# Kernel optimization log

Measured on AMD Instinct MI355X. Metric: run time of the kernel, lower is better.

The kernel has to match this reference:

```python
import jax, jax.numpy as jnp
import numpy as np
import math

C, NH, HD, L, P, FFN = 256, 8, 32, 1, 4, 512
H_BEV, W_BEV = 200, 100
NQ, BS, NV = 1000, 4, H_BEV * W_BEV
EPS = 1e-5


def _ln(x, g, b):
    m = x.mean(-1, keepdims=True)
    v = ((x - m) ** 2).mean(-1, keepdims=True)
    return (x - m) / jnp.sqrt(v + EPS) * g + b


def _mha(x, qpos, in_w, in_b, ow, ob):
    # nn.MultiheadAttention self-attention; key_pos = query_pos (shapes match)
    q = x + qpos
    k = x + qpos
    v = x
    wq, wk, wv = jnp.split(in_w, 3, axis=0)
    bq, bk, bv = jnp.split(in_b, 3, axis=0)
    bs, nq, _ = x.shape
    qh = (q @ wq.T + bq).reshape(bs, nq, NH, HD)
    kh = (k @ wk.T + bk).reshape(bs, nq, NH, HD)
    vh = (v @ wv.T + bv).reshape(bs, nq, NH, HD)
    scores = jnp.einsum('bqhd,bkhd->bhqk', qh, kh) / jnp.sqrt(jnp.float32(HD))
    attn = jax.nn.softmax(scores, axis=-1)
    out = jnp.einsum('bhqk,bkhd->bqhd', attn, vh).reshape(bs, nq, C)
    return out @ ow.T + ob


def _msdeform(x, qpos, value, ref, spatial_shapes, so_w, so_b, aw_w, aw_b, vp_w, vp_b, op_w, op_b):
    # Multi-scale deformable attention (single level), bilinear sampling with
    # align_corners=False convention and zero padding, as in the CUDA kernel.
    bs, nq, _ = x.shape
    q = x + qpos
    v = (value @ vp_w.T + vp_b).reshape(bs, NV, NH, HD).transpose(0, 2, 1, 3)  # [bs,nh,nv,hd]
    off = (q @ so_w.T + so_b).reshape(bs, nq, NH, L, P, 2)
    aw = jax.nn.softmax((q @ aw_w.T + aw_b).reshape(bs, nq, NH, L * P), axis=-1)
    aw = aw.reshape(bs, nq, NH, L, P)
    norm = jnp.stack([spatial_shapes[:, 1], spatial_shapes[:, 0]], -1).astype(jnp.float32)  # [L,2] = (W,H)
    loc = ref[:, :, None, :, None, :] + off / norm[None, None, None, :, None, :]  # [bs,nq,nh,L,P,2]
    loc = loc[:, :, :, 0]  # single level -> [bs,nq,nh,P,2]
    awp = aw[:, :, :, 0]   # [bs,nq,nh,P]
    x_im = loc[..., 0] * W_BEV - 0.5
    y_im = loc[..., 1] * H_BEV - 0.5
    x0 = jnp.floor(x_im)
    y0 = jnp.floor(y_im)
    lx = x_im - x0
    ly = y_im - y0
    x0i = x0.astype(jnp.int32)
    y0i = y0.astype(jnp.int32)
    acc = jnp.zeros((bs, NH, nq, P, HD), jnp.float32)
    for dy in (0, 1):
        for dx in (0, 1):
            xi = x0i + dx
            yi = y0i + dy
            w = (lx if dx else 1.0 - lx) * (ly if dy else 1.0 - ly)  # [bs,nq,nh,P]
            ok = ((xi >= 0) & (xi < W_BEV) & (yi >= 0) & (yi < H_BEV)).astype(jnp.float32)
            idx = jnp.clip(yi, 0, H_BEV - 1) * W_BEV + jnp.clip(xi, 0, W_BEV - 1)
            idx_t = idx.transpose(0, 2, 1, 3).reshape(bs, NH, nq * P)
            g = jnp.take_along_axis(v, idx_t[..., None], axis=2).reshape(bs, NH, nq, P, HD)
            acc = acc + g * (w * ok).transpose(0, 2, 1, 3)[..., None]
    out = (acc * awp.transpose(0, 2, 1, 3)[..., None]).sum(3)  # [bs,nh,nq,hd]
    out = out.transpose(0, 2, 1, 3).reshape(bs, nq, C)
    return out @ op_w.T + op_b


def setup_inputs() -> dict:
    key = jax.random.key(0)
    ks = jax.random.split(key, 24)
    f32 = jnp.float32

    def w(k, shp):
        fan = shp[-1]
        return (jax.random.normal(k, shp, f32) * (1.0 / np.sqrt(fan))).astype(f32)

    # sampling_offsets bias per _reset_parameters (radial grid init)
    thetas = np.arange(NH, dtype=np.float32) * (2.0 * math.pi / NH)
    grid = np.stack([np.cos(thetas), np.sin(thetas)], -1)
    grid = grid / np.abs(grid).max(-1, keepdims=True)
    grid = np.tile(grid[:, None, None, :], (1, L, P, 1))
    for i in range(P):
        grid[:, :, i, :] *= i + 1
    so_b = jnp.asarray(grid.reshape(-1), f32)

    return {
        'query': jax.random.normal(ks[0], (NQ, BS, C), f32),
        'value': jax.random.normal(ks[1], (NV, BS, C), f32),
        'query_pos': jax.random.normal(ks[2], (NQ, BS, C), f32),
        'reference_points': jax.random.uniform(ks[3], (BS, NQ, L, 2), f32),
        'spatial_shapes': jnp.array([[H_BEV, W_BEV]], jnp.int32),
        'level_start_index': jnp.zeros((L,), jnp.int32),
        'in_proj_w': w(ks[4], (3 * C, C)),
        'in_proj_b': jnp.zeros((3 * C,), f32),
        'mha_ow': w(ks[5], (C, C)),
        'mha_ob': jnp.zeros((C,), f32),
        'so_w': w(ks[6], (NH * L * P * 2, C)) * 0.01,
        'so_b': so_b,
        'aw_w': w(ks[7], (NH * L * P, C)) * 0.01,
        'aw_b': jnp.zeros((NH * L * P,), f32),
        'vp_w': w(ks[8], (C, C)),
        'vp_b': jnp.zeros((C,), f32),
        'op_w': w(ks[9], (C, C)),
        'op_b': jnp.zeros((C,), f32),
        'ffn_w1': w(ks[10], (FFN, C)),
        'ffn_b1': jnp.zeros((FFN,), f32),
        'ffn_w2': w(ks[11], (C, FFN)),
        'ffn_b2': jnp.zeros((C,), f32),
        'ln1_g': jnp.ones((C,), f32), 'ln1_b': jnp.zeros((C,), f32),
        'ln2_g': jnp.ones((C,), f32), 'ln2_b': jnp.zeros((C,), f32),
        'ln3_g': jnp.ones((C,), f32), 'ln3_b': jnp.zeros((C,), f32),
    }


def reference(query, value, query_pos, reference_points, spatial_shapes, level_start_index,
              in_proj_w, in_proj_b, mha_ow, mha_ob, so_w, so_b, aw_w, aw_b,
              vp_w, vp_b, op_w, op_b, ffn_w1, ffn_b1, ffn_w2, ffn_b2,
              ln1_g, ln1_b, ln2_g, ln2_b, ln3_g, ln3_b):
    # batch_first=False: (seq, bs, C) -> (bs, seq, C)
    x = query.transpose(1, 0, 2)
    val = value.transpose(1, 0, 2)
    qpos = query_pos.transpose(1, 0, 2)
    # self_attn -> norm (residual inside attn wrapper; dropout=0 in eval)
    x = _ln(x + _mha(x, qpos, in_proj_w, in_proj_b, mha_ow, mha_ob), ln1_g, ln1_b)
    # cross_attn (MSDeformAttn) -> norm
    x = _ln(x + _msdeform(x, qpos, val, reference_points, spatial_shapes,
                          so_w, so_b, aw_w, aw_b, vp_w, vp_b, op_w, op_b), ln2_g, ln2_b)
    # ffn -> norm
    h = jax.nn.relu(x @ ffn_w1.T + ffn_b1) @ ffn_w2.T + ffn_b2
    x = _ln(x + h, ln3_g, ln3_b)
    return x.transpose(1, 0, 2)
```

## Files before the change

### kernel.cpp

```cpp
#include <hip/hip_runtime.h>
#include <hip/hip_bf16.h>
#include <cmath>

#define BS   4
#define NQ   1000
#define CDIM 256
#define NH   8
#define HD   32
#define NVAL 20000
#define FFND 512
#define PN   4
#define WBEV 100
#define HBEV 200
#define TK   32

typedef __bf16 v8bf __attribute__((ext_vector_type(8)));
typedef float  v4f  __attribute__((ext_vector_type(4)));

__device__ __forceinline__ void gload_lds16(const void* g, void* l) {
    __builtin_amdgcn_global_load_lds(
        (const __attribute__((address_space(1))) unsigned int*)g,
        (__attribute__((address_space(3))) unsigned int*)l, 16, 0, 0);
}

__global__ __launch_bounds__(256) void prep_all_kernel(
    const float* __restrict__ query, const float* __restrict__ qpos,
    const float* __restrict__ in_w, const float* __restrict__ mha_ow,
    const float* __restrict__ vp_w, const float* __restrict__ op_w,
    const float* __restrict__ ffn_w1, const float* __restrict__ ffn_w2,
    const float* __restrict__ so_w, const float* __restrict__ aw_w,
    const float* __restrict__ so_b, const float* __restrict__ aw_b,
    float* __restrict__ x, float* __restrict__ qpos_t,
    __bf16* __restrict__ x_bf, __bf16* __restrict__ xq_bf,
    __bf16* __restrict__ wb, __bf16* __restrict__ wsmall,
    float* __restrict__ bsmall)
{
    int blk = blockIdx.x, tid = threadIdx.x;
    if (blk < 640) {
        long e = ((long)blk * 256 + tid) * 4;
        const float* src; long off;
        if      (e < 196608) { src = in_w;   off = e; }
        else if (e < 262144) { src = mha_ow; off = e - 196608; }
        else if (e < 327680) { src = vp_w;   off = e - 262144; }
        else if (e < 393216) { src = op_w;   off = e - 327680; }
        else if (e < 524288) { src = ffn_w1; off = e - 393216; }
        else                 { src = ffn_w2; off = e - 524288; }
        float4 v = *(const float4*)(src + off);
        __bf16* d = wb + e;
        d[0] = (__bf16)v.x; d[1] = (__bf16)v.y; d[2] = (__bf16)v.z; d[3] = (__bf16)v.w;
    } else if (blk < 4640) {
        int qb = blk - 640;
        int q = qb / BS, b = qb % BS;
        float qv = query[(q * BS + b) * CDIM + tid];
        float pv = qpos [(q * BS + b) * CDIM + tid];
        int o = (b * NQ + q) * CDIM + tid;
        x[o] = qv; qpos_t[o] = pv;
        x_bf[o] = (__bf16)qv; xq_bf[o] = (__bf16)(qv + pv);
    } else if (blk < 4672) {
        long e = ((long)(blk - 4640) * 256 + tid) * 4;
        int row = (int)(e >> 8), col = (int)(e & 255);
        float4 v = {0.f, 0.f, 0.f, 0.f};
        if (row < 64)      v = *(const float4*)(so_w + row * 256 + col);
        else if (row < 96) v = *(const float4*)(aw_w + (row - 64) * 256 + col);
        __bf16* d = wsmall + e;
        d[0] = (__bf16)v.x; d[1] = (__bf16)v.y; d[2] = (__bf16)v.z; d[3] = (__bf16)v.w;
    } else {
        if (tid < 128) bsmall[tid] = tid < 64 ? so_b[tid] : (tid < 96 ? aw_b[tid - 64] : 0.f);
    }
}

template<int TBM, int TBN>
__global__ __launch_bounds__(256) void mgemm_kernel(
    const __bf16* __restrict__ A, const __bf16* __restrict__ W,
    const float* __restrict__ bias, float* __restrict__ Yf,
    __bf16* __restrict__ Yb, int M, int N, int K, int relu)
{
    constexpr int WMF = TBM / 32;
    constexpr int WNF = TBN / 32;
    __shared__ __bf16 As[TBM][64];
    __shared__ __bf16 Bs[TBN][64];
    int bm = blockIdx.y * TBM, bn = blockIdx.x * TBN;
    int tid = threadIdx.x;
    int wave = tid >> 6, lane = tid & 63, quad = lane >> 4, n16 = lane & 15;
    int wm = (wave & 1) * (TBM / 2), wn = (wave >> 1) * (TBN / 2);
    v4f acc[WMF][WNF] = {};

    for (int k0 = 0; k0 < K; k0 += 64) {
        __syncthreads();
        #pragma unroll
        for (int i = 0; i < TBM * 8 / 256; i++) {
            int e = i * 256 + tid;
            int r = e >> 3, c = (e & 7) ^ (r & 7);
            int row = bm + r; if (row > M - 1) row = M - 1;
            gload_lds16(A + (long)row * K + k0 + c * 8, &As[0][0] + e * 8);
        }
        #pragma unroll
        for (int i = 0; i < TBN * 8 / 256; i++) {
            int e = i * 256 + tid;
            int r = e >> 3, c = (e & 7) ^ (r & 7);
            gload_lds16(W + (long)(bn + r) * K + k0 + c * 8, &Bs[0][0] + e * 8);
        }
        __syncthreads();
        #pragma unroll
        for (int s = 0; s < 2; s++) {
            v8bf af[WMF], bfr[WNF];
            #pragma unroll
            for (int mi = 0; mi < WMF; mi++) {
                int row = wm + mi * 16 + n16;
                af[mi] = *(v8bf*)&As[row][(((quad + s * 4) ^ (row & 7))) * 8];
            }
            #pragma unroll
            for (int nj = 0; nj < WNF; nj++) {
                int row = wn + nj * 16 + n16;
                bfr[nj] = *(v8bf*)&Bs[row][(((quad + s * 4) ^ (row & 7))) * 8];
            }
            #pragma unroll
            for (int mi = 0; mi < WMF; mi++)
                #pragma unroll
                for (int nj = 0; nj < WNF; nj++)
                    acc[mi][nj] = __builtin_amdgcn_mfma_f32_16x16x32_bf16(af[mi], bfr[nj], acc[mi][nj], 0, 0, 0);
        }
    }

    #pragma unroll
    for (int mi = 0; mi < WMF; mi++) {
        #pragma unroll
        for (int r = 0; r < 4; r++) {
            int m = bm + wm + mi * 16 + quad * 4 + r;
            if (m >= M) continue;
            #pragma unroll
            for (int nj = 0; nj < WNF; nj++) {
                int nn = bn + wn + nj * 16 + n16;
                if (nn >= N) continue;
                float v = acc[mi][nj][r] + bias[nn];
                if (relu) v = fmaxf(v, 0.f);
                if (Yf) Yf[(long)m * N + nn] = v;
                if (Yb) Yb[(long)m * N + nn] = (__bf16)v;
            }
        }
    }
}

__global__ __launch_bounds__(256) void vgemm_kernel(
    const float* __restrict__ A, const __bf16* __restrict__ W,
    const float* __restrict__ bias, __bf16* __restrict__ Yb)
{
    constexpr int TBM = 128, TBN = 128, WMF = 4, WNF = 4;
    __shared__ __bf16 As[TBM][64];
    __shared__ __bf16 Bs[TBN][64];
    int bm = blockIdx.y * TBM, bn = blockIdx.x * TBN;
    int tid = threadIdx.x;
    int wave = tid >> 6, lane = tid & 63, quad = lane >> 4, n16 = lane & 15;
    int wm = (wave & 1) * 64, wn = (wave >> 1) * 64;
    v4f acc[WMF][WNF] = {};

    for (int k0 = 0; k0 < 256; k0 += 64) {
        float4 fa[4][2];
        #pragma unroll
        for (int i = 0; i < 4; i++) {
            int e = i * 256 + tid;
            int r = e >> 3, c = (e & 7) ^ (r & 7);
            const float* p = A + (long)(bm + r) * 256 + k0 + c * 8;
            fa[i][0] = *(const float4*)p;
            fa[i][1] = *(const float4*)(p + 4);
        }
        __syncthreads();
        #pragma unroll
        for (int i = 0; i < 4; i++) {
            int e = i * 256 + tid;
            v8bf v;
            v[0] = (__bf16)fa[i][0].x; v[1] = (__bf16)fa[i][0].y;
            v[2] = (__bf16)fa[i][0].z; v[3] = (__bf16)fa[i][0].w;
            v[4] = (__bf16)fa[i][1].x; v[5] = (__bf16)fa[i][1].y;
            v[6] = (__bf16)fa[i][1].z; v[7] = (__bf16)fa[i][1].w;
            *(v8bf*)(&As[0][0] + e * 8) = v;
        }
        #pragma unroll
        for (int i = 0; i < 4; i++) {
            int e = i * 256 + tid;
            int r = e >> 3, c = (e & 7) ^ (r & 7);
            gload_lds16(W + (long)(bn + r) * 256 + k0 + c * 8, &Bs[0][0] + e * 8);
        }
        __syncthreads();
        #pragma unroll
        for (int s = 0; s < 2; s++) {
            v8bf af[WMF], bfr[WNF];
            #pragma unroll
            for (int mi = 0; mi < WMF; mi++) {
                int row = wm + mi * 16 + n16;
                af[mi] = *(v8bf*)&As[row][(((quad + s * 4) ^ (row & 7))) * 8];
            }
            #pragma unroll
            for (int nj = 0; nj < WNF; nj++) {
                int row = wn + nj * 16 + n16;
                bfr[nj] = *(v8bf*)&Bs[row][(((quad + s * 4) ^ (row & 7))) * 8];
            }
            #pragma unroll
            for (int mi = 0; mi < WMF; mi++)
                #pragma unroll
                for (int nj = 0; nj < WNF; nj++)
                    acc[mi][nj] = __builtin_amdgcn_mfma_f32_16x16x32_bf16(af[mi], bfr[nj], acc[mi][nj], 0, 0, 0);
        }
    }

    #pragma unroll
    for (int mi = 0; mi < WMF; mi++) {
        #pragma unroll
        for (int r = 0; r < 4; r++) {
            int m = bm + wm + mi * 16 + quad * 4 + r;
            #pragma unroll
            for (int nj = 0; nj < WNF; nj++) {
                int nn = bn + wn + nj * 16 + n16;
                Yb[(long)m * 256 + nn] = (__bf16)(acc[mi][nj][r] + bias[nn]);
            }
        }
    }
}

__global__ __launch_bounds__(256) void fattn_kernel(
    const __bf16* __restrict__ qk, const __bf16* __restrict__ vh,
    __bf16* __restrict__ out)
{
    __shared__ __bf16 Ks[2][TK][40];
    __shared__ __bf16 Vt[2][HD][40];
    __shared__ __bf16 Pl[4][16][40];
    int qt = blockIdx.x, h = blockIdx.y, b = blockIdx.z;
    int tid = threadIdx.x;
    int wave = tid >> 6, lane = tid & 63;
    int quad = lane >> 4, n = lane & 15;
    int q0 = qt * 64 + wave * 16;
    const float scale = 0.17677669529663687f;
    const float M0 = 8.0f;

    int qrow = q0 + n; if (qrow > NQ - 1) qrow = NQ - 1;
    v8bf aq = *(const v8bf*)(qk + (long)(b * NQ + qrow) * 512 + h * HD + quad * 8);

    v4f o0 = {}, o1 = {};
    float lp[4] = {0.f, 0.f, 0.f, 0.f};

    int sv = tid >> 7;
    int t2 = tid & 127;
    int key = t2 >> 2;
    int d8 = (t2 & 3) * 8;
    int vcol = key ^ (((d8 >> 3) & 1) << 4);

    auto loadtile = [&](int k0) -> v8bf {
        int krow = k0 + key; if (krow > NQ - 1) krow = NQ - 1;
        const __bf16* p = sv ? (vh + (long)(b * NQ + krow) * CDIM + h * HD + d8)
                             : (qk + (long)(b * NQ + krow) * 512 + 256 + h * HD + d8);
        return *(const v8bf*)p;
    };

    v8bf stg = loadtile(0);
    int pb = 0;
    for (int k0 = 0; k0 < NQ; k0 += TK) {
        if (sv == 0) {
            *(v8bf*)&Ks[pb][key][d8] = stg;
        } else {
            #pragma unroll
            for (int j = 0; j < 8; j++) Vt[pb][d8 + j][vcol] = stg[j];
        }
        if (k0 + TK < NQ) stg = loadtile(k0 + TK);
        __syncthreads();

        v8bf bk0 = *(v8bf*)&Ks[pb][n][quad * 8];
        v8bf bk1 = *(v8bf*)&Ks[pb][16 + n][quad * 8];
        v4f z = {};
        v4f S0 = __builtin_amdgcn_mfma_f32_16x16x32_bf16(aq, bk0, z, 0, 0, 0);
        v4f S1 = __builtin_amdgcn_mfma_f32_16x16x32_bf16(aq, bk1, z, 0, 0, 0);

        bool last = (k0 + TK > NQ);
        float p0[4], p1[4];
        #pragma unroll
        for (int r = 0; r < 4; r++) {
            p0[r] = __expf(fmaf(S0[r], scale, -M0));
            p1[r] = __expf(fmaf(S1[r], scale, -M0));
            if (last) {
                if (k0 + n >= NQ)      p0[r] = 0.f;
                if (k0 + 16 + n >= NQ) p1[r] = 0.f;
            }
            lp[r] += p0[r] + p1[r];
        }
        #pragma unroll
        for (int r = 0; r < 4; r++) {
            Pl[wave][quad * 4 + r][n]      = (__bf16)p0[r];
            Pl[wave][quad * 4 + r][16 + n] = (__bf16)p1[r];
        }
        asm volatile("s_waitcnt lgkmcnt(0)" ::: "memory");
        v8bf ap = *(v8bf*)&Pl[wave][n][quad * 8];
        int vc = (quad * 8) ^ (((n >> 3) & 1) << 4);
        v8bf bv0 = *(v8bf*)&Vt[pb][n][vc];
        v8bf bv1 = *(v8bf*)&Vt[pb][16 + n][vc];
        o0 = __builtin_amdgcn_mfma_f32_16x16x32_bf16(ap, bv0, o0, 0, 0, 0);
        o1 = __builtin_amdgcn_mfma_f32_16x16x32_bf16(ap, bv1, o1, 0, 0, 0);
        pb ^= 1;
    }

    #pragma unroll
    for (int r = 0; r < 4; r++) {
        float l = lp[r];
        #pragma unroll
        for (int off = 1; off < 16; off <<= 1) l += __shfl_xor(l, off, 16);
        int q = q0 + quad * 4 + r;
        if (q < NQ) {
            float invl = 1.0f / l;
            __bf16* op = out + ((long)(b * NQ + q) * CDIM + h * HD);
            op[n]      = (__bf16)(o0[r] * invl);
            op[16 + n] = (__bf16)(o1[r] * invl);
        }
    }
}

__global__ __launch_bounds__(256) void ln1q_kernel(
    const float* __restrict__ a, const float* __restrict__ bres,
    const float* __restrict__ g, const float* __restrict__ beta,
    const float* __restrict__ qpos_t,
    float* __restrict__ outf, __bf16* __restrict__ outq)
{
    int row = blockIdx.x, t = threadIdx.x;
    __shared__ float red[256];
    float v = a[(long)row * CDIM + t] + bres[(long)row * CDIM + t];
    red[t] = v; __syncthreads();
    for (int s = 128; s > 0; s >>= 1) { if (t < s) red[t] += red[t + s]; __syncthreads(); }
    float mean = red[0] * (1.0f / CDIM);
    __syncthreads();
    float dv = v - mean;
    red[t] = dv * dv; __syncthreads();
    for (int s = 128; s > 0; s >>= 1) { if (t < s) red[t] += red[t + s]; __syncthreads(); }
    float var = red[0] * (1.0f / CDIM);
    float r = rsqrtf(var + 1e-5f);
    float o = dv * r * g[t] + beta[t];
    outf[(long)row * CDIM + t] = o;
    outq[(long)row * CDIM + t] = (__bf16)(o + qpos_t[(long)row * CDIM + t]);
}

__global__ __launch_bounds__(256) void ln_kernel(
    const float* __restrict__ a, const float* __restrict__ bres,
    const float* __restrict__ g, const float* __restrict__ beta,
    float* __restrict__ outf, __bf16* __restrict__ outb)
{
    int row = blockIdx.x, t = threadIdx.x;
    __shared__ float red[256];
    float v = a[(long)row * CDIM + t] + bres[(long)row * CDIM + t];
    red[t] = v; __syncthreads();
    for (int s = 128; s > 0; s >>= 1) { if (t < s) red[t] += red[t + s]; __syncthreads(); }
    float mean = red[0] * (1.0f / CDIM);
    __syncthreads();
    float dv = v - mean;
    red[t] = dv * dv; __syncthreads();
    for (int s = 128; s > 0; s >>= 1) { if (t < s) red[t] += red[t + s]; __syncthreads(); }
    float var = red[0] * (1.0f / CDIM);
    float r = rsqrtf(var + 1e-5f);
    float o = dv * r * g[t] + beta[t];
    outf[(long)row * CDIM + t] = o;
    outb[(long)row * CDIM + t] = (__bf16)o;
}

__global__ __launch_bounds__(256) void ln3out_kernel(
    const float* __restrict__ a, const float* __restrict__ bres,
    const float* __restrict__ g, const float* __restrict__ beta,
    float* __restrict__ out)
{
    int row = blockIdx.x, t = threadIdx.x;
    int b = row / NQ, q = row % NQ;
    __shared__ float red[256];
    float v = a[(long)row * CDIM + t] + bres[(long)row * CDIM + t];
    red[t] = v; __syncthreads();
    for (int s = 128; s > 0; s >>= 1) { if (t < s) red[t] += red[t + s]; __syncthreads(); }
    float mean = red[0] * (1.0f / CDIM);
    __syncthreads();
    float dv = v - mean;
    red[t] = dv * dv; __syncthreads();
    for (int s = 128; s > 0; s >>= 1) { if (t < s) red[t] += red[t + s]; __syncthreads(); }
    float var = red[0] * (1.0f / CDIM);
    float r = rsqrtf(var + 1e-5f);
    out[(long)(q * BS + b) * CDIM + t] = dv * r * g[t] + beta[t];
}

__global__ __launch_bounds__(256) void msds_kernel(
    const __bf16* __restrict__ vproj, const float* __restrict__ soaw,
    const float* __restrict__ refp, __bf16* __restrict__ out)
{
    int bq = blockIdx.x; int b = bq / NQ; int q = bq % NQ;
    int t = threadIdx.x; int h = t / HD; int d = t % HD;
    float rx = refp[(b * NQ + q) * 2 + 0];
    float ry = refp[(b * NQ + q) * 2 + 1];
    const float* rowp = soaw + (long)(b * NQ + q) * 96;
    const float* offp = rowp + h * 8;
    const float* awp  = rowp + 64 + h * 4;
    float a0 = awp[0], a1 = awp[1], a2 = awp[2], a3 = awp[3];
    float m = fmaxf(fmaxf(a0, a1), fmaxf(a2, a3));
    float e0 = __expf(a0 - m), e1 = __expf(a1 - m), e2 = __expf(a2 - m), e3 = __expf(a3 - m);
    float invs = 1.0f / (e0 + e1 + e2 + e3);
    float acc = 0.f;
    #pragma unroll
    for (int p = 0; p < PN; p++) {
        float ew = (p == 0 ? e0 : p == 1 ? e1 : p == 2 ? e2 : e3) * invs;
        float xim = rx * (float)WBEV + offp[p * 2 + 0] - 0.5f;
        float yim = ry * (float)HBEV + offp[p * 2 + 1] - 0.5f;
        float x0f = floorf(xim), y0f = floorf(yim);
        float lx = xim - x0f, ly = yim - y0f;
        int x0 = (int)x0f, y0 = (int)y0f;
        float gsum = 0.f;
        #pragma unroll
        for (int dy = 0; dy < 2; dy++) {
            #pragma unroll
            for (int dx = 0; dx < 2; dx++) {
                int xi = x0 + dx, yi = y0 + dy;
                float w = (dx ? lx : 1.f - lx) * (dy ? ly : 1.f - ly);
                bool ok = (xi >= 0 && xi < WBEV && yi >= 0 && yi < HBEV);
                int xc = min(max(xi, 0), WBEV - 1);
                int yc = min(max(yi, 0), HBEV - 1);
                int idx = yc * WBEV + xc;
                float gv = (float)vproj[((long)(idx * BS + b)) * CDIM + h * HD + d];
                gsum += (ok ? w : 0.f) * gv;
            }
        }
        acc += ew * gsum;
    }
    out[(b * NQ + q) * CDIM + h * HD + d] = (__bf16)acc;
}

extern "C" void kernel_launch(void* const* d_in, const int* in_sizes, int n_in,
                              void* d_out, int out_size, void* d_ws, size_t ws_size,
                              hipStream_t stream) {
    const float* query = (const float*)d_in[0];
    const float* value = (const float*)d_in[1];
    const float* qpos  = (const float*)d_in[2];
    const float* refp  = (const float*)d_in[3];
    const float* in_w  = (const float*)d_in[6];
    const float* in_b  = (const float*)d_in[7];
    const float* mha_ow = (const float*)d_in[8];
    const float* mha_ob = (const float*)d_in[9];
    const float* so_w  = (const float*)d_in[10];
    const float* so_b  = (const float*)d_in[11];
    const float* aw_w  = (const float*)d_in[12];
    const float* aw_b  = (const float*)d_in[13];
    const float* vp_w  = (const float*)d_in[14];
    const float* vp_b  = (const float*)d_in[15];
    const float* op_w  = (const float*)d_in[16];
    const float* op_b  = (const float*)d_in[17];
    const float* ffn_w1 = (const float*)d_in[18];
    const float* ffn_b1 = (const float*)d_in[19];
    const float* ffn_w2 = (const float*)d_in[20];
    const float* ffn_b2 = (const float*)d_in[21];
    const float* ln1_g = (const float*)d_in[22];
    const float* ln1_b = (const float*)d_in[23];
    const float* ln2_g = (const float*)d_in[24];
    const float* ln2_b = (const float*)d_in[25];
    const float* ln3_g = (const float*)d_in[26];
    const float* ln3_b = (const float*)d_in[27];
    float* out = (float*)d_out;

    const long NTOK = (long)BS * NQ * CDIM;

    float* x      = (float*)d_ws;
    float* qpos_t = x + NTOK;
    float* bufB   = qpos_t + NTOK;
    float* x1     = bufB + NTOK;
    float* x2     = x1 + NTOK;
    float* soaw   = x2 + NTOK;
    float* bsmall = soaw + (long)BS * NQ * 96;
    __bf16* x_bf   = (__bf16*)(bsmall + 128);
    __bf16* xq_bf  = x_bf + NTOK;
    __bf16* qk_bf  = xq_bf + NTOK;
    __bf16* vh_bf  = qk_bf + 2 * NTOK;
    __bf16* aA_bf  = vh_bf + NTOK;
    __bf16* x2_bf  = aA_bf + NTOK;
    __bf16* h1_bf  = x2_bf + NTOK;
    __bf16* vpj_bf = h1_bf + 2 * NTOK;
    __bf16* wb     = vpj_bf + (long)BS * NVAL * CDIM;
    __bf16* inw_b  = wb;
    __bf16* mow_b  = wb + 196608;
    __bf16* vpw_b  = wb + 262144;
    __bf16* opw_b  = wb + 327680;
    __bf16* fw1_b  = wb + 393216;
    __bf16* fw2_b  = wb + 524288;
    __bf16* wsmall = wb + 655360;

    const int M = BS * NQ;
    dim3 blk(256);

    prep_all_kernel<<<4673, blk, 0, stream>>>(
        query, qpos, in_w, mha_ow, vp_w, op_w, ffn_w1, ffn_w2,
        so_w, aw_w, so_b, aw_b,
        x, qpos_t, x_bf, xq_bf, wb, wsmall, bsmall);

    mgemm_kernel<64,64><<<dim3(8, 63), blk, 0, stream>>>(xq_bf, inw_b,          in_b,       nullptr, qk_bf, M, 512, 256, 0);
    mgemm_kernel<64,64><<<dim3(4, 63), blk, 0, stream>>>(x_bf,  inw_b + 131072, in_b + 512, nullptr, vh_bf, M, 256, 256, 0);

    fattn_kernel<<<dim3((NQ + 63) / 64, NH, BS), blk, 0, stream>>>(qk_bf, vh_bf, aA_bf);

    mgemm_kernel<64,64><<<dim3(4, 63), blk, 0, stream>>>(aA_bf, mow_b, mha_ob, bufB, nullptr, M, 256, 256, 0);

    ln1q_kernel<<<M, blk, 0, stream>>>(x, bufB, ln1_g, ln1_b, qpos_t, x1, xq_bf);

    mgemm_kernel<64,128><<<dim3(1, 63), blk, 0, stream>>>(xq_bf, wsmall, bsmall, soaw, nullptr, M, 96, 256, 0);

    vgemm_kernel<<<dim3(2, 625), blk, 0, stream>>>(value, vpw_b, vp_b, vpj_bf);

    msds_kernel<<<M, blk, 0, stream>>>(vpj_bf, soaw, refp, aA_bf);

    mgemm_kernel<64,64><<<dim3(4, 63), blk, 0, stream>>>(aA_bf, opw_b, op_b, bufB, nullptr, M, 256, 256, 0);

    ln_kernel<<<M, blk, 0, stream>>>(x1, bufB, ln2_g, ln2_b, x2, x2_bf);

    mgemm_kernel<64,64><<<dim3(8, 63), blk, 0, stream>>>(x2_bf, fw1_b, ffn_b1, nullptr, h1_bf, M, 512, 256, 1);
    mgemm_kernel<64,64><<<dim3(4, 63), blk, 0, stream>>>(h1_bf, fw2_b, ffn_b2, bufB, nullptr, M, 256, 512, 0);

    ln3out_kernel<<<M, blk, 0, stream>>>(x2, bufB, ln3_g, ln3_b, out);
}
```

Measured before the change: 307.6 us.

## Fuse output GEMMs with residual LayerNorm and merge QKV projections

The three LayerNorm kernels are folded into the preceding 256-wide output GEMMs. Each block computes a full 16-row stripe, then does the residual add, bias and row statistics in-register. This removes the fp32 intermediate buffer round trip and three launches. The Q/K and V projections also become one launch, and the sampling-offset GEMM uses a smaller M tile. The risks are that only 250 blocks run the fused GEMMs, each loading the full weight matrix per K step, and that the one-pass variance is less numerically stable.

```diff
diff --git a/kernel.cpp b/kernel.cpp
--- a/kernel.cpp
+++ b/kernel.cpp
@@ -141,14 +141,180 @@
     }
 }
 
+__global__ __launch_bounds__(256) void qkv_kernel(
+    const __bf16* __restrict__ xq, const __bf16* __restrict__ xv,
+    const __bf16* __restrict__ W, const float* __restrict__ bias,
+    __bf16* __restrict__ qk, __bf16* __restrict__ vh)
+{
+    __shared__ __bf16 As[64][64];
+    __shared__ __bf16 Bs[64][64];
+    int bm = blockIdx.y * 64, bn = blockIdx.x * 64;
+    const __bf16* A = (bn < 512) ? xq : xv;
+    int tid = threadIdx.x;
+    int wave = tid >> 6, lane = tid & 63, quad = lane >> 4, n16 = lane & 15;
+    int wm = (wave & 1) * 32, wn = (wave >> 1) * 32;
+    v4f acc[2][2] = {};
+
+    for (int k0 = 0; k0 < 256; k0 += 64) {
+        __syncthreads();
+        #pragma unroll
+        for (int i = 0; i < 2; i++) {
+            int e = i * 256 + tid;
+            int r = e >> 3, c = (e & 7) ^ (r & 7);
+            int row = bm + r; if (row > BS * NQ - 1) row = BS * NQ - 1;
+            gload_lds16(A + (long)row * 256 + k0 + c * 8, &As[0][0] + e * 8);
+        }
+        #pragma unroll
+        for (int i = 0; i < 2; i++) {
+            int e = i * 256 + tid;
+            int r = e >> 3, c = (e & 7) ^ (r & 7);
+            gload_lds16(W + (long)(bn + r) * 256 + k0 + c * 8, &Bs[0][0] + e * 8);
+        }
+        __syncthreads();
+        #pragma unroll
+        for (int s = 0; s < 2; s++) {
+            v8bf af[2], bfr[2];
+            #pragma unroll
+            for (int mi = 0; mi < 2; mi++) {
+                int row = wm + mi * 16 + n16;
+                af[mi] = *(v8bf*)&As[row][(((quad + s * 4) ^ (row & 7))) * 8];
+            }
+            #pragma unroll
+            for (int nj = 0; nj < 2; nj++) {
+                int row = wn + nj * 16 + n16;
+                bfr[nj] = *(v8bf*)&Bs[row][(((quad + s * 4) ^ (row & 7))) * 8];
+            }
+            #pragma unroll
+            for (int mi = 0; mi < 2; mi++)
+                #pragma unroll
+                for (int nj = 0; nj < 2; nj++)
+                    acc[mi][nj] = __builtin_amdgcn_mfma_f32_16x16x32_bf16(af[mi], bfr[nj], acc[mi][nj], 0, 0, 0);
+        }
+    }
+
+    #pragma unroll
+    for (int mi = 0; mi < 2; mi++) {
+        #pragma unroll
+        for (int r = 0; r < 4; r++) {
+            int m = bm + wm + mi * 16 + quad * 4 + r;
+            if (m >= BS * NQ) continue;
+            #pragma unroll
+            for (int nj = 0; nj < 2; nj++) {
+                int nn = bn + wn + nj * 16 + n16;
+                float v = acc[mi][nj][r] + bias[nn];
+                if (nn < 512) qk[(long)m * 512 + nn] = (__bf16)v;
+                else          vh[(long)m * 256 + (nn - 512)] = (__bf16)v;
+            }
+        }
+    }
+}
+
+template<int KD, int MODE>
+__global__ __launch_bounds__(256) void gemmln_kernel(
+    const __bf16* __restrict__ A, const __bf16* __restrict__ W,
+    const float* __restrict__ bias, const float* __restrict__ res,
+    const float* __restrict__ g, const float* __restrict__ beta,
+    const float* __restrict__ qpos_t,
+    float* __restrict__ outf, __bf16* __restrict__ outb)
+{
+    __shared__ __bf16 As[16][64];
+    __shared__ __bf16 Bs[256][64];
+    __shared__ float redS[4][16], redQ[4][16];
+    int bm = blockIdx.x * 16;
+    int tid = threadIdx.x;
+    int wave = tid >> 6, lane = tid & 63, quad = lane >> 4, n16 = lane & 15;
+    int wn = wave * 64;
+    v4f acc[4] = {};
+
+    for (int k0 = 0; k0 < KD; k0 += 64) {
+        __syncthreads();
+        if (tid < 128) {
+            int e = tid;
+            int r = e >> 3, c = (e & 7) ^ (r & 7);
+            gload_lds16(A + (long)(bm + r) * KD + k0 + c * 8, &As[0][0] + e * 8);
+        }
+        #pragma unroll
+        for (int i = 0; i < 8; i++) {
+            int e = i * 256 + tid;
+            int r = e >> 3, c = (e & 7) ^ (r & 7);
+            gload_lds16(W + (long)r * KD + k0 + c * 8, &Bs[0][0] + e * 8);
+        }
+        __syncthreads();
+        #pragma unroll
+        for (int s = 0; s < 2; s++) {
+            v8bf af = *(v8bf*)&As[n16][(((quad + s * 4) ^ (n16 & 7))) * 8];
+            #pragma unroll
+            for (int nj = 0; nj < 4; nj++) {
+                int row = wn + nj * 16 + n16;
+                v8bf bfr = *(v8bf*)&Bs[row][(((quad + s * 4) ^ (row & 7))) * 8];
+                acc[nj] = __builtin_amdgcn_mfma_f32_16x16x32_bf16(af, bfr, acc[nj], 0, 0, 0);
+            }
+        }
+    }
+
+    float y[4][4], s1[4] = {}, s2[4] = {};
+    #pragma unroll
+    for (int r = 0; r < 4; r++) {
+        int m = bm + quad * 4 + r;
+        #pragma unroll
+        for (int nj = 0; nj < 4; nj++) {
+            int nn = wn + nj * 16 + n16;
+            float v = acc[nj][r] + bias[nn] + res[(long)m * 256 + nn];
+            y[r][nj] = v;
+            s1[r] += v; s2[r] += v * v;
+        }
+    }
+    #pragma unroll
+    for (int r = 0; r < 4; r++) {
+        #pragma unroll
+        for (int off = 1; off < 16; off <<= 1) {
+            s1[r] += __shfl_xor(s1[r], off, 16);
+            s2[r] += __shfl_xor(s2[r], off, 16);
+        }
+    }
+    if (n16 == 0) {
+        #pragma unroll
+        for (int r = 0; r < 4; r++) {
+            redS[wave][quad * 4 + r] = s1[r];
+            redQ[wave][quad * 4 + r] = s2[r];
+        }
+    }
+    __syncthreads();
+    #pragma unroll
+    for (int r = 0; r < 4; r++) {
+        int mr = quad * 4 + r;
+        float ts = redS[0][mr] + redS[1][mr] + redS[2][mr] + redS[3][mr];
+        float tq = redQ[0][mr] + redQ[1][mr] + redQ[2][mr] + redQ[3][mr];
+        float mean = ts * (1.0f / 256.0f);
+        float var = tq * (1.0f / 256.0f) - mean * mean;
+        float rinv = rsqrtf(var + 1e-5f);
+        int m = bm + mr;
+        #pragma unroll
+        for (int nj = 0; nj < 4; nj++) {
+            int nn = wn + nj * 16 + n16;
+            float o = (y[r][nj] - mean) * rinv * g[nn] + beta[nn];
+            if (MODE == 0) {
+                outf[(long)m * 256 + nn] = o;
+                outb[(long)m * 256 + nn] = (__bf16)(o + qpos_t[(long)m * 256 + nn]);
+            } else if (MODE == 1) {
+                outf[(long)m * 256 + nn] = o;
+                outb[(long)m * 256 + nn] = (__bf16)o;
+            } else {
+                int b = m / NQ, q = m % NQ;
+                outf[(long)(q * BS + b) * 256 + nn] = o;
+            }
+        }
+    }
+}
+
 __global__ __launch_bounds__(256) void vgemm_kernel(
     const float* __restrict__ A, const __bf16* __restrict__ W,
     const float* __restrict__ bias, __bf16* __restrict__ Yb)
 {
-    constexpr int TBM = 128, TBN = 128, WMF = 4, WNF = 4;
-    __shared__ __bf16 As[TBM][64];
-    __shared__ __bf16 Bs[TBN][64];
-    int bm = blockIdx.y * TBM, bn = blockIdx.x * TBN;
+    constexpr int WMF = 4, WNF = 4;
+    __shared__ __bf16 As[128][64];
+    __shared__ __bf16 Bs[128][64];
+    int bm = blockIdx.y * 128, bn = blockIdx.x * 128;
     int tid = threadIdx.x;
     int wave = tid >> 6, lane = tid & 63, quad = lane >> 4, n16 = lane & 15;
     int wm = (wave & 1) * 64, wn = (wave >> 1) * 64;
@@ -309,72 +475,6 @@
             op[16 + n] = (__bf16)(o1[r] * invl);
         }
     }
-}
-
-__global__ __launch_bounds__(256) void ln1q_kernel(
-    const float* __restrict__ a, const float* __restrict__ bres,
-    const float* __restrict__ g, const float* __restrict__ beta,
-    const float* __restrict__ qpos_t,
-    float* __restrict__ outf, __bf16* __restrict__ outq)
-{
-    int row = blockIdx.x, t = threadIdx.x;
-    __shared__ float red[256];
-    float v = a[(long)row * CDIM + t] + bres[(long)row * CDIM + t];
-    red[t] = v; __syncthreads();
-    for (int s = 128; s > 0; s >>= 1) { if (t < s) red[t] += red[t + s]; __syncthreads(); }
-    float mean = red[0] * (1.0f / CDIM);
-    __syncthreads();
-    float dv = v - mean;
-    red[t] = dv * dv; __syncthreads();
-    for (int s = 128; s > 0; s >>= 1) { if (t < s) red[t] += red[t + s]; __syncthreads(); }
-    float var = red[0] * (1.0f / CDIM);
-    float r = rsqrtf(var + 1e-5f);
-    float o = dv * r * g[t] + beta[t];
-    outf[(long)row * CDIM + t] = o;
-    outq[(long)row * CDIM + t] = (__bf16)(o + qpos_t[(long)row * CDIM + t]);
-}
-
-__global__ __launch_bounds__(256) void ln_kernel(
-    const float* __restrict__ a, const float* __restrict__ bres,
-    const float* __restrict__ g, const float* __restrict__ beta,
-    float* __restrict__ outf, __bf16* __restrict__ outb)
-{
-    int row = blockIdx.x, t = threadIdx.x;
-    __shared__ float red[256];
-    float v = a[(long)row * CDIM + t] + bres[(long)row * CDIM + t];
-    red[t] = v; __syncthreads();
-    for (int s = 128; s > 0; s >>= 1) { if (t < s) red[t] += red[t + s]; __syncthreads(); }
-    float mean = red[0] * (1.0f / CDIM);
-    __syncthreads();
-    float dv = v - mean;
-    red[t] = dv * dv; __syncthreads();
-    for (int s = 128; s > 0; s >>= 1) { if (t < s) red[t] += red[t + s]; __syncthreads(); }
-    float var = red[0] * (1.0f / CDIM);
-    float r = rsqrtf(var + 1e-5f);
-    float o = dv * r * g[t] + beta[t];
-    outf[(long)row * CDIM + t] = o;
-    outb[(long)row * CDIM + t] = (__bf16)o;
-}
-
-__global__ __launch_bounds__(256) void ln3out_kernel(
-    const float* __restrict__ a, const float* __restrict__ bres,
-    const float* __restrict__ g, const float* __restrict__ beta,
-    float* __restrict__ out)
-{
-    int row = blockIdx.x, t = threadIdx.x;
-    int b = row / NQ, q = row % NQ;
-    __shared__ float red[256];
-    float v = a[(long)row * CDIM + t] + bres[(long)row * CDIM + t];
-    red[t] = v; __syncthreads();
-    for (int s = 128; s > 0; s >>= 1) { if (t < s) red[t] += red[t + s]; __syncthreads(); }
-    float mean = red[0] * (1.0f / CDIM);
-    __syncthreads();
-    float dv = v - mean;
-    red[t] = dv * dv; __syncthreads();
-    for (int s = 128; s > 0; s >>= 1) { if (t < s) red[t] += red[t + s]; __syncthreads(); }
-    float var = red[0] * (1.0f / CDIM);
-    float r = rsqrtf(var + 1e-5f);
-    out[(long)(q * BS + b) * CDIM + t] = dv * r * g[t] + beta[t];
 }
 
 __global__ __launch_bounds__(256) void msds_kernel(
@@ -456,8 +556,7 @@
 
     float* x      = (float*)d_ws;
     float* qpos_t = x + NTOK;
-    float* bufB   = qpos_t + NTOK;
-    float* x1     = bufB + NTOK;
+    float* x1     = qpos_t + NTOK;
     float* x2     = x1 + NTOK;
     float* soaw   = x2 + NTOK;
     float* bsmall = soaw + (long)BS * NQ * 96;
@@ -486,27 +585,26 @@
         so_w, aw_w, so_b, aw_b,
         x, qpos_t, x_bf, xq_bf, wb, wsmall, bsmall);
 
-    mgemm_kernel<64,64><<<dim3(8, 63), blk, 0, stream>>>(xq_bf, inw_b,          in_b,       nullptr, qk_bf, M, 512, 256, 0);
-    mgemm_kernel<64,64><<<dim3(4, 63), blk, 0, stream>>>(x_bf,  inw_b + 131072, in_b + 512, nullptr, vh_bf, M, 256, 256, 0);
+    qkv_kernel<<<dim3(12, 63), blk, 0, stream>>>(xq_bf, x_bf, inw_b, in_b, qk_bf, vh_bf);
 
     fattn_kernel<<<dim3((NQ + 63) / 64, NH, BS), blk, 0, stream>>>(qk_bf, vh_bf, aA_bf);
 
-    mgemm_kernel<64,64><<<dim3(4, 63), blk, 0, stream>>>(aA_bf, mow_b, mha_ob, bufB, nullptr, M, 256, 256, 0);
-
-    ln1q_kernel<<<M, blk, 0, stream>>>(x, bufB, ln1_g, ln1_b, qpos_t, x1, xq_bf);
-
-    mgemm_kernel<64,128><<<dim3(1, 63), blk, 0, stream>>>(xq_bf, wsmall, bsmall, soaw, nullptr, M, 96, 256, 0);
+    gemmln_kernel<256, 0><<<250, blk, 0, stream>>>(
+        aA_bf, mow_b, mha_ob, x, ln1_g, ln1_b, qpos_t, x1, xq_bf);
+
+    mgemm_kernel<32, 128><<<dim3(1, 125), blk, 0, stream>>>(
+        xq_bf, wsmall, bsmall, soaw, nullptr, M, 96, 256, 0);
 
     vgemm_kernel<<<dim3(2, 625), blk, 0, stream>>>(value, vpw_b, vp_b, vpj_bf);
 
     msds_kernel<<<M, blk, 0, stream>>>(vpj_bf, soaw, refp, aA_bf);
 
-    mgemm_kernel<64,64><<<dim3(4, 63), blk, 0, stream>>>(aA_bf, opw_b, op_b, bufB, nullptr, M, 256, 256, 0);
-
-    ln_kernel<<<M, blk, 0, stream>>>(x1, bufB, ln2_g, ln2_b, x2, x2_bf);
-
-    mgemm_kernel<64,64><<<dim3(8, 63), blk, 0, stream>>>(x2_bf, fw1_b, ffn_b1, nullptr, h1_bf, M, 512, 256, 1);
-    mgemm_kernel<64,64><<<dim3(4, 63), blk, 0, stream>>>(h1_bf, fw2_b, ffn_b2, bufB, nullptr, M, 256, 512, 0);
-
-    ln3out_kernel<<<M, blk, 0, stream>>>(x2, bufB, ln3_g, ln3_b, out);
-}
+    gemmln_kernel<256, 1><<<250, blk, 0, stream>>>(
+        aA_bf, opw_b, op_b, x1, ln2_g, ln2_b, nullptr, x2, x2_bf);
+
+    mgemm_kernel<64, 64><<<dim3(8, 63), blk, 0, stream>>>(
+        x2_bf, fw1_b, ffn_b1, nullptr, h1_bf, M, 512, 256, 1);
+
+    gemmln_kernel<512, 2><<<250, blk, 0, stream>>>(
+        h1_bf, fw2_b, ffn_b2, x2, ln3_g, ln3_b, nullptr, out, nullptr);
+}
```

Result: faster. 279.9 us (-9.0%).
